# Performance work log

Hardware: AMD Instinct MI355X
Metric: run time of the kernel (lower is better)

The kernel has to match this reference:

```python
import jax, jax.numpy as jnp
import numpy as np

B = 64       # number of graphs
R = 148      # fixed ROI count from source
D = 64       # hidden_channels (embed_dim, 4 heads)
H = 4
IN1 = 64     # node feature dim (after stripping label column)
INR = 148    # roi-graph feature dim
HID = 1000
NCLS = 2
N1 = 262144
E1 = 1048576
N2 = B * R
E2 = 262144
EPS = 1e-5


def setup_inputs() -> dict:
    key = jax.random.key(0)
    ks = jax.random.split(key, 40)
    def p(i, shape, s=0.1):
        return jax.random.normal(ks[i], shape, dtype=jnp.float32) * s
    inp = {
        'x_feat': jax.random.normal(ks[0], (N1, IN1), dtype=jnp.float32),
        'node_roi': jax.random.randint(ks[1], (N1,), 0, R, dtype=jnp.int32),
        'batch1': ((jnp.arange(N1, dtype=jnp.int32) * B) // N1).astype(jnp.int32),
        'edge_index1': jax.random.randint(ks[2], (2, E1), 0, N1, dtype=jnp.int32),
        'edge_weight1': jax.random.uniform(ks[3], (E1,), dtype=jnp.float32, minval=0.1, maxval=1.0),
        'x2_feat': jax.random.normal(ks[4], (N2, INR), dtype=jnp.float32),
        'roi_labels2': (jnp.arange(N2, dtype=jnp.int32) % R).astype(jnp.int32),
        'batch2': (jnp.arange(N2, dtype=jnp.int32) // R).astype(jnp.int32),
        'edge_index2': jax.random.randint(ks[5], (2, E2), 0, N2, dtype=jnp.int32),
        'edge_weight2': jax.random.uniform(ks[6], (E2,), dtype=jnp.float32, minval=0.1, maxval=1.0),
        'Wg1': p(7, (IN1, D)), 'bg1': jnp.zeros((D,), jnp.float32),
        'Wg2': p(8, (D, D)), 'bg2': jnp.zeros((D,), jnp.float32),
        'Wr1': p(9, (INR, D)), 'br1': jnp.zeros((D,), jnp.float32),
        'Wr2': p(10, (D, D)), 'br2': jnp.zeros((D,), jnp.float32),
        'in_proj_w': p(11, (3 * D, D)), 'in_proj_b': jnp.zeros((3 * D,), jnp.float32),
        'out_proj_w': p(12, (D, D)), 'out_proj_b': jnp.zeros((D,), jnp.float32),
        'ln1_g': jnp.ones((D,), jnp.float32), 'ln1_b': jnp.zeros((D,), jnp.float32),
        'ff_w1': p(13, (D, D)), 'ff_b1': jnp.zeros((D,), jnp.float32),
        'ff_w2': p(14, (D, D)), 'ff_b2': jnp.zeros((D,), jnp.float32),
        'ln2_g': jnp.ones((D,), jnp.float32), 'ln2_b': jnp.zeros((D,), jnp.float32),
        'Wc1': p(15, (R * D, HID), 0.02), 'bc1': jnp.zeros((HID,), jnp.float32),
        'bn_g': jnp.ones((HID,), jnp.float32), 'bn_b': jnp.zeros((HID,), jnp.float32),
        'Wc2': p(16, (HID, NCLS), 0.02), 'bc2': jnp.zeros((NCLS,), jnp.float32),
    }
    return inp


def gcn_conv(h, src, dst, ew, W, b, n):
    # PyG GCNConv w/ edge weights: add self-loops (weight 1), sym-normalize.
    h = h @ W
    deg = jax.ops.segment_sum(ew, dst, num_segments=n) + 1.0
    dinv = jax.lax.rsqrt(deg)
    norm = dinv[src] * ew * dinv[dst]                      # (E,)
    agg = jax.ops.segment_sum(h[src] * norm[:, None], dst, num_segments=n)
    agg = agg + h * (dinv * dinv)[:, None]                 # self-loop term
    return agg + b


def roi_pool_mean(h, roi, batch):
    # fused scatter mean keyed by (batch, roi) -> (B, R, d); empty slots stay 0
    seg = batch * R + roi
    sums = jax.ops.segment_sum(h, seg, num_segments=B * R)
    cnt = jax.ops.segment_sum(jnp.ones_like(h[:, 0]), seg, num_segments=B * R)
    return (sums / jnp.maximum(cnt, 1.0)[:, None]).reshape(B, R, h.shape[1])


def layer_norm(x, g, b):
    mu = x.mean(axis=-1, keepdims=True)
    var = x.var(axis=-1, keepdims=True)
    return (x - mu) * jax.lax.rsqrt(var + EPS) * g + b


def reference(x_feat, node_roi, batch1, edge_index1, edge_weight1,
              x2_feat, roi_labels2, batch2, edge_index2, edge_weight2,
              Wg1, bg1, Wg2, bg2, Wr1, br1, Wr2, br2,
              in_proj_w, in_proj_b, out_proj_w, out_proj_b,
              ln1_g, ln1_b, ff_w1, ff_b1, ff_w2, ff_b2, ln2_g, ln2_b,
              Wc1, bc1, bn_g, bn_b, Wc2, bc2):
    s1, d1 = edge_index1[0], edge_index1[1]
    s2, d2 = edge_index2[0], edge_index2[1]

    # ROI-graph branch (convs_roi[:-1]): 2 GCN layers, relu, eval dropout=noop
    h2 = jax.nn.relu(gcn_conv(x2_feat, s2, d2, edge_weight2, Wr1, br1, N2))
    h2 = jax.nn.relu(gcn_conv(h2, s2, d2, edge_weight2, Wr2, br2, N2))
    pooled_roi = roi_pool_mean(h2, roi_labels2, batch2)          # (B,R,D)

    # node-graph branch (convs[:-1])
    h1 = jax.nn.relu(gcn_conv(x_feat, s1, d1, edge_weight1, Wg1, bg1, N1))
    h1 = jax.nn.relu(gcn_conv(h1, s1, d1, edge_weight1, Wg2, bg2, N1))
    pooled = roi_pool_mean(h1, node_roi, batch1)                 # (B,R,D)

    combined = pooled + pooled_roi                               # transformer_in_combined

    # SelfAttnBlock (torch MultiheadAttention, batch_first, 4 heads)
    hd = D // H
    qkv = combined @ in_proj_w.T + in_proj_b                     # (B,R,3D)
    q, k, v = jnp.split(qkv, 3, axis=-1)
    q = q.reshape(B, R, H, hd)
    k = k.reshape(B, R, H, hd)
    v = v.reshape(B, R, H, hd)
    scores = jnp.einsum('bqhd,bkhd->bhqk', q, k) / np.sqrt(hd).astype(np.float32)
    attn_w = jax.nn.softmax(scores, axis=-1)                     # (B,H,R,R)
    o = jnp.einsum('bhqk,bkhd->bqhd', attn_w, v).reshape(B, R, D)
    o = o @ out_proj_w.T + out_proj_b
    x = layer_norm(combined + o, ln1_g, ln1_b)
    f = jax.nn.relu(x @ ff_w1 + ff_b1) @ ff_w2 + ff_b2
    t_out = layer_norm(x + f, ln2_g, ln2_b)                      # (B,R,D)

    # classifier: Linear -> BatchNorm1d(eval: mean0,var1) -> LeakyReLU -> Linear
    z = t_out.reshape(B, R * D) @ Wc1 + bc1
    z = bn_g * z * jax.lax.rsqrt(jnp.asarray(1.0 + EPS, z.dtype)) + bn_b
    z = jnp.where(z >= 0, z, 0.01 * z)
    out = z @ Wc2 + bc2                                          # (B,NCLS)
    return (out, pooled, pooled_roi, t_out, attn_w)
```

## Files before the change

### kernel.cpp

```cpp
#include <hip/hip_runtime.h>
#include <cstdint>
#include <cstddef>

#define N1v 262144
#define E1v 1048576
#define N2v 9472
#define E2v 262144
#define BBv 64
#define RRv 148
#define HIDv 1000
#define BRv (BBv * RRv)
#define NSEG 9472
#define EPB 4096
#define NBK1 256
#define SH1 10
#define BINS1 1024
#define CAP1 4864
#define NBK2 74
#define SH2 7
#define BINS2 128
#define CAP2 4096

__host__ __device__ constexpr int cdiv(int a, int b) { return (a + b - 1) / b; }

typedef __attribute__((ext_vector_type(8))) short bf16x8;
typedef __attribute__((ext_vector_type(4))) float f32x4;
typedef unsigned short ushort_t;
typedef unsigned long long u64;

__device__ inline short f2bf(float f) {
    union { float f; unsigned u; } v; v.f = f;
    unsigned r = v.u + 0x7fff + ((v.u >> 16) & 1);
    return (short)(r >> 16);
}
__device__ inline float bf2f(unsigned hs) {
    union { unsigned u; float f; } v; v.u = hs << 16; return v.f;
}
__device__ inline unsigned relu_pk(unsigned u) {
    unsigned r = u;
    if (r & 0x8000u) r &= 0xFFFF0000u;
    if (r & 0x80000000u) r &= 0x0000FFFFu;
    return r;
}

__global__ __launch_bounds__(256) void k_binA(const int* __restrict__ dst1, int* __restrict__ bc1,
                                              const int* __restrict__ dst2, int* __restrict__ bc2) {
    int bid = blockIdx.x;
    const int* dst; int* bc; int nbk, sh, e0;
    if (bid < E1v / EPB) { dst = dst1; bc = bc1; nbk = NBK1; sh = SH1; e0 = bid * EPB; }
    else { dst = dst2; bc = bc2; nbk = NBK2; sh = SH2; e0 = (bid - E1v / EPB) * EPB; }
    __shared__ int h[256];
    int tid = threadIdx.x;
    if (tid < nbk) h[tid] = 0;
    __syncthreads();
    for (int t = tid; t < EPB; t += 256) atomicAdd(&h[dst[e0 + t] >> sh], 1);
    __syncthreads();
    if (tid < nbk && h[tid]) atomicAdd(&bc[tid], h[tid]);
}

__global__ __launch_bounds__(256) void k_scanAB(const int* __restrict__ bc1, int* __restrict__ bb1, int* __restrict__ cur1,
                                                const int* __restrict__ bc2, int* __restrict__ bb2, int* __restrict__ cur2) {
    __shared__ int tmp[256];
    int t = threadIdx.x;
    int v = bc1[t];
    tmp[t] = v; __syncthreads();
    int val = v;
    for (int off = 1; off < 256; off <<= 1) { int o = (t >= off) ? tmp[t - off] : 0; __syncthreads(); val += o; tmp[t] = val; __syncthreads(); }
    int excl = val - v;
    bb1[t] = excl; cur1[t] = excl;
    if (t == 255) bb1[256] = val;
    __syncthreads();
    int v2 = (t < NBK2) ? bc2[t] : 0;
    tmp[t] = v2; __syncthreads();
    int val2 = v2;
    for (int off = 1; off < 256; off <<= 1) { int o = (t >= off) ? tmp[t - off] : 0; __syncthreads(); val2 += o; tmp[t] = val2; __syncthreads(); }
    if (t < NBK2) { int e2 = val2 - v2; bb2[t] = e2; cur2[t] = e2; }
    if (t == NBK2 - 1) bb2[NBK2] = val2;
}

__global__ __launch_bounds__(256) void k_binB(const int* __restrict__ src1, const int* __restrict__ dst1,
                                              const float* __restrict__ ew1, int* __restrict__ cur1, u64* __restrict__ rb1,
                                              const int* __restrict__ src2, const int* __restrict__ dst2,
                                              const float* __restrict__ ew2, int* __restrict__ cur2, u64* __restrict__ rb2) {
    int bid = blockIdx.x;
    const int* src; const int* dst; const float* ew; int* cur; u64* rb; int nbk, sh, e0;
    if (bid < E1v / EPB) { src = src1; dst = dst1; ew = ew1; cur = cur1; rb = rb1; nbk = NBK1; sh = SH1; e0 = bid * EPB; }
    else { src = src2; dst = dst2; ew = ew2; cur = cur2; rb = rb2; nbk = NBK2; sh = SH2; e0 = (bid - E1v / EPB) * EPB; }
    __shared__ int h[256], basg[256];
    int tid = threadIdx.x;
    if (tid < nbk) h[tid] = 0;
    __syncthreads();
    for (int t = tid; t < EPB; t += 256) atomicAdd(&h[dst[e0 + t] >> sh], 1);
    __syncthreads();
    if (tid < nbk) {
        int c = h[tid];
        basg[tid] = c ? atomicAdd(&cur[tid], c) : 0;
        h[tid] = 0;
    }
    __syncthreads();
    unsigned lowmask = (1u << sh) - 1u;
    for (int t = tid; t < EPB; t += 256) {
        int d = dst[e0 + t];
        int b = d >> sh;
        int r = atomicAdd(&h[b], 1);
        unsigned lo = ((unsigned)src[e0 + t] << sh) | ((unsigned)d & lowmask);
        rb[(size_t)basg[b] + r] = ((u64)(unsigned)__float_as_int(ew[e0 + t]) << 32) | lo;
    }
}

template<int BINS, int CAP, int SH>
__global__ __launch_bounds__(256) void k_csrC(const u64* __restrict__ rb, const int* __restrict__ bb,
                                              float* __restrict__ dinv, int* __restrict__ offs,
                                              int2* __restrict__ snC) {
    int b = blockIdx.x;
    int beg = bb[b], end = bb[b + 1], cnt = end - beg;
    __shared__ int hist[BINS];
    __shared__ float degs[BINS];
    __shared__ int scn[BINS];
    __shared__ int tmp[256];
    extern __shared__ int2 outb[];
    int tid = threadIdx.x;
    for (int i = tid; i < BINS; i += 256) { hist[i] = 0; degs[i] = 0.f; }
    __syncthreads();
    for (int j = beg + tid; j < end; j += 256) {
        u64 rec = rb[j];
        int bin = (int)((unsigned)rec & (BINS - 1));
        float w = __int_as_float((int)(rec >> 32));
        atomicAdd(&hist[bin], 1);
        atomicAdd(&degs[bin], w);
    }
    __syncthreads();
    constexpr int PER = (BINS + 255) / 256;
    int lv[PER];
    int tsum = 0;
    int base_i = tid * PER;
#pragma unroll
    for (int k = 0; k < PER; ++k) { int idx = base_i + k; lv[k] = (idx < BINS) ? hist[idx] : 0; tsum += lv[k]; }
    tmp[tid] = tsum; __syncthreads();
    int val = tsum;
    for (int off = 1; off < 256; off <<= 1) { int o = (tid >= off) ? tmp[tid - off] : 0; __syncthreads(); val += o; tmp[tid] = val; __syncthreads(); }
    int run = val - tsum;
#pragma unroll
    for (int k = 0; k < PER; ++k) { int idx = base_i + k; if (idx < BINS) { scn[idx] = run; run += lv[k]; } }
    __syncthreads();
    for (int i = tid; i < BINS; i += 256) {
        offs[b * BINS + i] = beg + scn[i];
        dinv[b * BINS + i] = rsqrtf(degs[i] + 1.0f);
    }
    __syncthreads();
    bool staged = (cnt <= CAP);
    for (int j = beg + tid; j < end; j += 256) {
        u64 rec = rb[j];
        unsigned lo = (unsigned)rec;
        int bin = (int)(lo & (BINS - 1));
        int s = (int)(lo >> SH);
        int wbits = (int)(rec >> 32);
        int r = atomicAdd(&scn[bin], 1);
        int2 o2 = make_int2(s, wbits);
        if (staged) outb[r] = o2;
        else snC[(size_t)beg + r] = o2;
    }
    __syncthreads();
    if (staged) {
        for (int j = tid; j < cnt; j += 256) snC[(size_t)beg + j] = outb[j];
    }
}

__global__ __launch_bounds__(256) void k_pool_csr(const int* __restrict__ roi, int* __restrict__ offs_p,
                                                  int* __restrict__ nodeC) {
    int b = blockIdx.x;
    __shared__ int rl[4096];
    __shared__ int hist[RRv];
    __shared__ int curs[RRv];
    int tid = threadIdx.x;
    for (int t = tid; t < RRv; t += 256) hist[t] = 0;
    __syncthreads();
    int base = b * 4096;
    for (int t = tid; t < 4096; t += 256) {
        int r = roi[base + t];
        rl[t] = r;
        atomicAdd(&hist[r], 1);
    }
    __syncthreads();
    if (tid < RRv) {
        int s = 0;
        for (int k = 0; k < tid; ++k) s += hist[k];
        curs[tid] = s;
        offs_p[b * RRv + tid] = base + s;
    }
    __syncthreads();
    for (int t = tid; t < 4096; t += 256) {
        int r = rl[t];
        int j = atomicAdd(&curs[r], 1);
        nodeC[base + j] = base + t;
    }
}

__global__ __launch_bounds__(256) void k_pool_gather(const int* __restrict__ nodeC, const int* __restrict__ offs,
                                                     const ushort_t* __restrict__ Ab, float* __restrict__ pooled) {
    int tid = threadIdx.x;
    int lane = tid & 63;
    int nh = lane >> 5;
    int slot = (lane >> 3) & 3;
    int f8 = lane & 7;
    int gw = blockIdx.x * 4 + (tid >> 6);
    int tw = gridDim.x * 4;
    for (int ss = gw * 2; ss < NSEG; ss += tw * 2) {
        int s = ss + nh;
        int beg = offs[s];
        int end = (s + 1 < NSEG) ? offs[s + 1] : N1v;
        float a0 = 0.f, a1 = 0.f, a2 = 0.f, a3 = 0.f, a4 = 0.f, a5 = 0.f, a6 = 0.f, a7 = 0.f;
        for (int j = beg + slot; j < end; j += 4) {
            int node = nodeC[j];
            uint4 v = *(const uint4*)(Ab + (size_t)node * 64 + f8 * 8);
            a0 += fmaxf(bf2f(v.x & 0xffffu), 0.f);
            a1 += fmaxf(bf2f(v.x >> 16), 0.f);
            a2 += fmaxf(bf2f(v.y & 0xffffu), 0.f);
            a3 += fmaxf(bf2f(v.y >> 16), 0.f);
            a4 += fmaxf(bf2f(v.z & 0xffffu), 0.f);
            a5 += fmaxf(bf2f(v.z >> 16), 0.f);
            a6 += fmaxf(bf2f(v.w & 0xffffu), 0.f);
            a7 += fmaxf(bf2f(v.w >> 16), 0.f);
        }
        a0 += __shfl_xor(a0, 8);  a1 += __shfl_xor(a1, 8);  a2 += __shfl_xor(a2, 8);  a3 += __shfl_xor(a3, 8);
        a4 += __shfl_xor(a4, 8);  a5 += __shfl_xor(a5, 8);  a6 += __shfl_xor(a6, 8);  a7 += __shfl_xor(a7, 8);
        a0 += __shfl_xor(a0, 16); a1 += __shfl_xor(a1, 16); a2 += __shfl_xor(a2, 16); a3 += __shfl_xor(a3, 16);
        a4 += __shfl_xor(a4, 16); a5 += __shfl_xor(a5, 16); a6 += __shfl_xor(a6, 16); a7 += __shfl_xor(a7, 16);
        if (slot == 0) {
            float inv = 1.f / (float)max(end - beg, 1);
            float4 r0, r1;
            r0.x = a0 * inv; r0.y = a1 * inv; r0.z = a2 * inv; r0.w = a3 * inv;
            r1.x = a4 * inv; r1.y = a5 * inv; r1.z = a6 * inv; r1.w = a7 * inv;
            *(float4*)(pooled + (size_t)s * 64 + f8 * 8) = r0;
            *(float4*)(pooled + (size_t)s * 64 + f8 * 8 + 4) = r1;
        }
    }
}

__global__ __launch_bounds__(256) void k_edge_gather3(const int2* __restrict__ snC,
                                                      const int* __restrict__ offs, const ushort_t* __restrict__ Pb,
                                                      const float* __restrict__ dinv, const float* __restrict__ bias,
                                                      ushort_t* __restrict__ A, int N, int E) {
    int tid = threadIdx.x;
    int lane = tid & 63;
    int nh = lane >> 5;
    int slot = (lane >> 3) & 3;
    int f8 = lane & 7;
    float4 bv0 = *(const float4*)(bias + f8 * 8);
    float4 bv1 = *(const float4*)(bias + f8 * 8 + 4);
    int gw = blockIdx.x * 4 + (tid >> 6);
    int tw = gridDim.x * 4;
    for (int ii = gw * 2; ii < N; ii += tw * 2) {
        int i = ii + nh;
        int beg = offs[i];
        int end = (i + 1 < N) ? offs[i + 1] : E;
        float di = dinv[i];
        float a0 = 0.f, a1 = 0.f, a2 = 0.f, a3 = 0.f, a4 = 0.f, a5 = 0.f, a6 = 0.f, a7 = 0.f;
        for (int j = beg + slot; j < end; j += 4) {
            int2 e = snC[j];
            int s = e.x;
            float nv = dinv[s] * __int_as_float(e.y) * di;
            uint4 w = *(const uint4*)(Pb + (size_t)s * 64 + f8 * 8);
            a0 = fmaf(nv, bf2f(w.x & 0xffffu), a0);
            a1 = fmaf(nv, bf2f(w.x >> 16), a1);
            a2 = fmaf(nv, bf2f(w.y & 0xffffu), a2);
            a3 = fmaf(nv, bf2f(w.y >> 16), a3);
            a4 = fmaf(nv, bf2f(w.z & 0xffffu), a4);
            a5 = fmaf(nv, bf2f(w.z >> 16), a5);
            a6 = fmaf(nv, bf2f(w.w & 0xffffu), a6);
            a7 = fmaf(nv, bf2f(w.w >> 16), a7);
        }
        a0 += __shfl_xor(a0, 8);  a1 += __shfl_xor(a1, 8);  a2 += __shfl_xor(a2, 8);  a3 += __shfl_xor(a3, 8);
        a4 += __shfl_xor(a4, 8);  a5 += __shfl_xor(a5, 8);  a6 += __shfl_xor(a6, 8);  a7 += __shfl_xor(a7, 8);
        a0 += __shfl_xor(a0, 16); a1 += __shfl_xor(a1, 16); a2 += __shfl_xor(a2, 16); a3 += __shfl_xor(a3, 16);
        a4 += __shfl_xor(a4, 16); a5 += __shfl_xor(a5, 16); a6 += __shfl_xor(a6, 16); a7 += __shfl_xor(a7, 16);
        if (slot == 0) {
            uint4 w = *(const uint4*)(Pb + (size_t)i * 64 + f8 * 8);
            float s2 = di * di;
            float r0 = fmaf(s2, bf2f(w.x & 0xffffu), a0) + bv0.x;
            float r1 = fmaf(s2, bf2f(w.x >> 16),    a1) + bv0.y;
            float r2 = fmaf(s2, bf2f(w.y & 0xffffu), a2) + bv0.z;
            float r3 = fmaf(s2, bf2f(w.y >> 16),    a3) + bv0.w;
            float r4 = fmaf(s2, bf2f(w.z & 0xffffu), a4) + bv1.x;
            float r5 = fmaf(s2, bf2f(w.z >> 16),    a5) + bv1.y;
            float r6 = fmaf(s2, bf2f(w.w & 0xffffu), a6) + bv1.z;
            float r7 = fmaf(s2, bf2f(w.w >> 16),    a7) + bv1.w;
            uint4 ov;
            ov.x = (unsigned)(ushort_t)f2bf(r0) | ((unsigned)(ushort_t)f2bf(r1) << 16);
            ov.y = (unsigned)(ushort_t)f2bf(r2) | ((unsigned)(ushort_t)f2bf(r3) << 16);
            ov.z = (unsigned)(ushort_t)f2bf(r4) | ((unsigned)(ushort_t)f2bf(r5) << 16);
            ov.w = (unsigned)(ushort_t)f2bf(r6) | ((unsigned)(ushort_t)f2bf(r7) << 16);
            *(uint4*)(A + (size_t)i * 64 + f8 * 8) = ov;
        }
    }
}

template<bool RIN, bool IBF16>
__global__ __launch_bounds__(256) void k_gemm_mfma(const void* __restrict__ Xv, const float* __restrict__ Wmat,
                                                   ushort_t* __restrict__ Y, int N) {
    int tid = threadIdx.x;
    int lane = tid & 63;
    int wv = tid >> 6;
    int l15 = lane & 15;
    int lg = lane >> 4;
    bf16x8 bfrag[2][4];
    for (int kh = 0; kh < 2; ++kh)
        for (int ct = 0; ct < 4; ++ct) {
            bf16x8 b;
#pragma unroll
            for (int i = 0; i < 8; ++i)
                b[i] = f2bf(Wmat[(size_t)(kh * 32 + lg * 8 + i) * 64 + ct * 16 + l15]);
            bfrag[kh][ct] = b;
        }
    int gw = blockIdx.x * 4 + wv;
    int tw = gridDim.x * 4;
    int ntiles = N >> 4;
    for (int t = gw; t < ntiles; t += tw) {
        int row0 = t << 4;
        bf16x8 af0, af1;
        if (IBF16) {
            const ushort_t* xp = (const ushort_t*)Xv + (size_t)(row0 + l15) * 64 + lg * 8;
            uint4 c0 = *(const uint4*)(xp);
            uint4 c1 = *(const uint4*)(xp + 32);
            if (RIN) {
                c0.x = relu_pk(c0.x); c0.y = relu_pk(c0.y); c0.z = relu_pk(c0.z); c0.w = relu_pk(c0.w);
                c1.x = relu_pk(c1.x); c1.y = relu_pk(c1.y); c1.z = relu_pk(c1.z); c1.w = relu_pk(c1.w);
            }
            af0 = *reinterpret_cast<bf16x8*>(&c0);
            af1 = *reinterpret_cast<bf16x8*>(&c1);
        } else {
            const float* xp = (const float*)Xv + (size_t)(row0 + l15) * 64 + lg * 8;
            float4 a0 = *(const float4*)(xp);
            float4 a1 = *(const float4*)(xp + 4);
            float4 a2 = *(const float4*)(xp + 32);
            float4 a3 = *(const float4*)(xp + 36);
            if (RIN) {
                a0.x = fmaxf(a0.x, 0.f); a0.y = fmaxf(a0.y, 0.f); a0.z = fmaxf(a0.z, 0.f); a0.w = fmaxf(a0.w, 0.f);
                a1.x = fmaxf(a1.x, 0.f); a1.y = fmaxf(a1.y, 0.f); a1.z = fmaxf(a1.z, 0.f); a1.w = fmaxf(a1.w, 0.f);
                a2.x = fmaxf(a2.x, 0.f); a2.y = fmaxf(a2.y, 0.f); a2.z = fmaxf(a2.z, 0.f); a2.w = fmaxf(a2.w, 0.f);
                a3.x = fmaxf(a3.x, 0.f); a3.y = fmaxf(a3.y, 0.f); a3.z = fmaxf(a3.z, 0.f); a3.w = fmaxf(a3.w, 0.f);
            }
            af0[0] = f2bf(a0.x); af0[1] = f2bf(a0.y); af0[2] = f2bf(a0.z); af0[3] = f2bf(a0.w);
            af0[4] = f2bf(a1.x); af0[5] = f2bf(a1.y); af0[6] = f2bf(a1.z); af0[7] = f2bf(a1.w);
            af1[0] = f2bf(a2.x); af1[1] = f2bf(a2.y); af1[2] = f2bf(a2.z); af1[3] = f2bf(a2.w);
            af1[4] = f2bf(a3.x); af1[5] = f2bf(a3.y); af1[6] = f2bf(a3.z); af1[7] = f2bf(a3.w);
        }
        f32x4 acc0 = {0.f, 0.f, 0.f, 0.f}, acc1 = acc0, acc2 = acc0, acc3 = acc0;
        acc0 = __builtin_amdgcn_mfma_f32_16x16x32_bf16(af0, bfrag[0][0], acc0, 0, 0, 0);
        acc1 = __builtin_amdgcn_mfma_f32_16x16x32_bf16(af0, bfrag[0][1], acc1, 0, 0, 0);
        acc2 = __builtin_amdgcn_mfma_f32_16x16x32_bf16(af0, bfrag[0][2], acc2, 0, 0, 0);
        acc3 = __builtin_amdgcn_mfma_f32_16x16x32_bf16(af0, bfrag[0][3], acc3, 0, 0, 0);
        acc0 = __builtin_amdgcn_mfma_f32_16x16x32_bf16(af1, bfrag[1][0], acc0, 0, 0, 0);
        acc1 = __builtin_amdgcn_mfma_f32_16x16x32_bf16(af1, bfrag[1][1], acc1, 0, 0, 0);
        acc2 = __builtin_amdgcn_mfma_f32_16x16x32_bf16(af1, bfrag[1][2], acc2, 0, 0, 0);
        acc3 = __builtin_amdgcn_mfma_f32_16x16x32_bf16(af1, bfrag[1][3], acc3, 0, 0, 0);
        ushort_t* yp = Y + (size_t)(row0 + lg * 4) * 64 + l15;
#pragma unroll
        for (int r = 0; r < 4; ++r) {
            yp[(size_t)r * 64 + 0]  = (ushort_t)f2bf(acc0[r]);
            yp[(size_t)r * 64 + 16] = (ushort_t)f2bf(acc1[r]);
            yp[(size_t)r * 64 + 32] = (ushort_t)f2bf(acc2[r]);
            yp[(size_t)r * 64 + 48] = (ushort_t)f2bf(acc3[r]);
        }
    }
}

template<int MB, bool RIN, bool ROUT, bool OBF16>
__global__ __launch_bounds__(256) void k_gemm_rowwave(const float* __restrict__ X, const float* __restrict__ W,
                                                      const float* __restrict__ bias, void* __restrict__ Yv,
                                                      int N, int K) {
    extern __shared__ float Wl[];
    const int M = MB * 64;
    for (int idx = threadIdx.x; idx < K * M; idx += 256) Wl[idx] = W[idx];
    __syncthreads();
    int lane = threadIdx.x & 63;
    int gw = blockIdx.x * 4 + (threadIdx.x >> 6);
    int tw = gridDim.x * 4;
    const int K4 = K >> 2;
    for (int row = gw; row < N; row += tw) {
        float acc[MB];
#pragma unroll
        for (int cb = 0; cb < MB; ++cb) acc[cb] = 0.f;
        const float4* xr = (const float4*)(X + (size_t)row * K);
        for (int k4 = 0; k4 < K4; ++k4) {
            float4 xv = xr[k4];
            if (RIN) {
                xv.x = fmaxf(xv.x, 0.f); xv.y = fmaxf(xv.y, 0.f);
                xv.z = fmaxf(xv.z, 0.f); xv.w = fmaxf(xv.w, 0.f);
            }
            const float* wp = Wl + (k4 * 4) * M + lane;
#pragma unroll
            for (int cb = 0; cb < MB; ++cb) acc[cb] = fmaf(xv.x, wp[cb * 64], acc[cb]);
            wp += M;
#pragma unroll
            for (int cb = 0; cb < MB; ++cb) acc[cb] = fmaf(xv.y, wp[cb * 64], acc[cb]);
            wp += M;
#pragma unroll
            for (int cb = 0; cb < MB; ++cb) acc[cb] = fmaf(xv.z, wp[cb * 64], acc[cb]);
            wp += M;
#pragma unroll
            for (int cb = 0; cb < MB; ++cb) acc[cb] = fmaf(xv.w, wp[cb * 64], acc[cb]);
        }
#pragma unroll
        for (int cb = 0; cb < MB; ++cb) {
            float y = acc[cb];
            int col = cb * 64 + lane;
            if (bias) y += bias[col];
            if (ROUT) y = fmaxf(y, 0.f);
            if (OBF16) ((ushort_t*)Yv)[(size_t)row * M + col] = (ushort_t)f2bf(y);
            else ((float*)Yv)[(size_t)row * M + col] = y;
        }
    }
}

__global__ __launch_bounds__(256) void k_transpose2(const float* __restrict__ Win, float* __restrict__ WinT,
                                                    const float* __restrict__ Wout, float* __restrict__ WoutT) {
    int i = blockIdx.x * 256 + threadIdx.x;
    if (i < 192 * 64) {
        int r = i >> 6, c = i & 63;
        WinT[c * 192 + r] = Win[i];
    } else if (i < 192 * 64 + 64 * 64) {
        int j = i - 192 * 64;
        int r = j >> 6, c = j & 63;
        WoutT[c * 64 + r] = Wout[j];
    }
}

__global__ __launch_bounds__(256) void k_pool_fin2b(const ushort_t* __restrict__ h2Ab, const float* __restrict__ pooled,
                                                    float* __restrict__ pooledroi, float* __restrict__ comb,
                                                    int n4) {
    int i = blockIdx.x * 256 + threadIdx.x;
    if (i < n4) {
        uint2 v = *(const uint2*)(h2Ab + (size_t)i * 4);
        float4 p = ((const float4*)pooled)[i];
        float4 r;
        r.x = fmaxf(bf2f(v.x & 0xffffu), 0.f);
        r.y = fmaxf(bf2f(v.x >> 16), 0.f);
        r.z = fmaxf(bf2f(v.y & 0xffffu), 0.f);
        r.w = fmaxf(bf2f(v.y >> 16), 0.f);
        ((float4*)pooledroi)[i] = r;
        float4 c;
        c.x = r.x + p.x; c.y = r.y + p.y; c.z = r.z + p.z; c.w = r.w + p.w;
        ((float4*)comb)[i] = c;
    }
}

__global__ __launch_bounds__(256) void k_attn(const float* __restrict__ qkv, float* __restrict__ aw,
                                              float* __restrict__ o) {
    int qc = blockIdx.x & 3;
    int bh = blockIdx.x >> 2;
    int b = bh >> 2, h = bh & 3;
    __shared__ float qs[37][16];
    __shared__ float kT[16][152];
    __shared__ float vs[148][16];
    __shared__ float ps[4][152];
    int tid = threadIdx.x;
    const float* base = qkv + (size_t)b * 148 * 192 + h * 16;
    for (int idx = tid; idx < 148 * 16; idx += 256) {
        int i = idx >> 4, d = idx & 15;
        const float* p = base + (size_t)i * 192 + d;
        kT[d][i] = p[64];
        vs[i][d] = p[128];
    }
    int q0 = qc * 37;
    for (int idx = tid; idx < 37 * 16; idx += 256) {
        int i = idx >> 4, d = idx & 15;
        qs[i][d] = base[(size_t)(q0 + i) * 192 + d] * 0.25f;
    }
    __syncthreads();
    int wv = tid >> 6, lane = tid & 63;
    float* aw_bh = aw + (size_t)bh * 148 * 148;
    for (int ii = wv; ii < 37; ii += 4) {
        int i = q0 + ii;
        float s0 = 0.f, s1 = 0.f, s2 = 0.f;
#pragma unroll
        for (int d = 0; d < 16; ++d) {
            float q = qs[ii][d];
            s0 = fmaf(q, kT[d][lane], s0);
            s1 = fmaf(q, kT[d][lane + 64], s1);
            if (lane < 20) s2 = fmaf(q, kT[d][lane + 128], s2);
        }
        float m = fmaxf(s0, s1);
        if (lane < 20) m = fmaxf(m, s2);
#pragma unroll
        for (int off = 1; off < 64; off <<= 1) m = fmaxf(m, __shfl_xor(m, off));
        float e0 = __expf(s0 - m), e1 = __expf(s1 - m);
        float e2 = (lane < 20) ? __expf(s2 - m) : 0.f;
        float sum = e0 + e1 + e2;
#pragma unroll
        for (int off = 1; off < 64; off <<= 1) sum += __shfl_xor(sum, off);
        float inv = 1.f / sum;
        float p0 = e0 * inv, p1 = e1 * inv, p2 = e2 * inv;
        float* awr = aw_bh + (size_t)i * 148;
        awr[lane] = p0;
        awr[lane + 64] = p1;
        if (lane < 20) awr[lane + 128] = p2;
        ps[wv][lane] = p0;
        ps[wv][lane + 64] = p1;
        if (lane < 20) ps[wv][lane + 128] = p2;
        int d = lane & 15, jj = lane >> 4;
        float acc = 0.f;
        for (int t = jj; t < 148; t += 4) acc = fmaf(ps[wv][t], vs[t][d], acc);
        acc += __shfl_xor(acc, 16);
        acc += __shfl_xor(acc, 32);
        if (lane < 16) o[((size_t)b * 148 + i) * 64 + h * 16 + d] = acc;
    }
}

__global__ __launch_bounds__(256) void k_ln_gemm(const float* __restrict__ X, const float* __restrict__ Wt,
                                                 const float* __restrict__ bias, const float* __restrict__ resid,
                                                 const float* __restrict__ g, const float* __restrict__ bb,
                                                 float* __restrict__ Y, int N) {
    __shared__ float Wl[4096];
    for (int idx = threadIdx.x; idx < 4096; idx += 256) Wl[idx] = Wt[idx];
    __syncthreads();
    int lane = threadIdx.x & 63;
    int gw = blockIdx.x * 4 + (threadIdx.x >> 6);
    int tw = gridDim.x * 4;
    for (int row = gw; row < N; row += tw) {
        const float4* xr = (const float4*)(X + (size_t)row * 64);
        float acc = 0.f;
        for (int k4 = 0; k4 < 16; ++k4) {
            float4 xv = xr[k4];
            const float* wp = Wl + (k4 * 4) * 64 + lane;
            acc = fmaf(xv.x, wp[0], acc);
            acc = fmaf(xv.y, wp[64], acc);
            acc = fmaf(xv.z, wp[128], acc);
            acc = fmaf(xv.w, wp[192], acc);
        }
        float y = acc + bias[lane] + resid[(size_t)row * 64 + lane];
        float s = y;
#pragma unroll
        for (int off = 1; off < 64; off <<= 1) s += __shfl_xor(s, off);
        float mu = s * (1.f / 64.f);
        float dcen = y - mu;
        float v = dcen * dcen;
#pragma unroll
        for (int off = 1; off < 64; off <<= 1) v += __shfl_xor(v, off);
        float var = v * (1.f / 64.f);
        Y[(size_t)row * 64 + lane] = dcen * rsqrtf(var + 1e-5f) * g[lane] + bb[lane];
    }
}

__global__ __launch_bounds__(256) void k_cls_part(const float* __restrict__ T, const float* __restrict__ Wc1,
                                                  float* __restrict__ Zp) {
    int ks = blockIdx.x >> 2;
    int mt = blockIdx.x & 3;
    int k0 = ks * 74;
    int m0 = mt * 256;
    __shared__ float Tl[64][74];
    int tid = threadIdx.x;
    for (int idx = tid; idx < 64 * 74; idx += 256) {
        int b = idx / 74, kk = idx - b * 74;
        Tl[b][kk] = T[(size_t)b * 9472 + k0 + kk];
    }
    __syncthreads();
    int lane = tid & 63, bq = tid >> 6;
    int mbase = m0 + lane * 4;
    size_t moff = (mbase + 3 < 1000) ? (size_t)mbase : 0;
    float4 acc[16];
#pragma unroll
    for (int j = 0; j < 16; ++j) acc[j] = make_float4(0.f, 0.f, 0.f, 0.f);
#pragma unroll 2
    for (int kk = 0; kk < 74; ++kk) {
        float4 w = *(const float4*)(Wc1 + (size_t)(k0 + kk) * 1000 + moff);
#pragma unroll
        for (int j = 0; j < 16; ++j) {
            float t = Tl[bq * 16 + j][kk];
            acc[j].x = fmaf(t, w.x, acc[j].x);
            acc[j].y = fmaf(t, w.y, acc[j].y);
            acc[j].z = fmaf(t, w.z, acc[j].z);
            acc[j].w = fmaf(t, w.w, acc[j].w);
        }
    }
    float* zp = Zp + (size_t)ks * 64 * 1024;
#pragma unroll
    for (int j = 0; j < 16; ++j) {
        int b = bq * 16 + j;
        *(float4*)(zp + (size_t)b * 1024 + mbase) = acc[j];
    }
}

__global__ __launch_bounds__(256) void k_cls_reduce(const float* __restrict__ Zp, const float* __restrict__ bc1,
                                                    const float* __restrict__ bn_g, const float* __restrict__ bn_b,
                                                    float* __restrict__ zb) {
    int flat = blockIdx.x * 256 + threadIdx.x;
    int b = flat >> 10, m = flat & 1023;
    if (m >= 1000) return;
    float s = 0.f;
    for (int ks = 0; ks < 128; ++ks)
        s += Zp[((size_t)ks * 64 + b) * 1024 + m];
    float rs = rsqrtf(1.0f + 1e-5f);
    float z = bn_g[m] * (s + bc1[m]) * rs + bn_b[m];
    zb[flat] = z >= 0.f ? z : 0.01f * z;
}

__global__ __launch_bounds__(256) void k_cls_final(const float* __restrict__ zb,
                                                   const float* __restrict__ Wc2, const float* __restrict__ bc2,
                                                   float* __restrict__ out) {
    int b = blockIdx.x;
    int tid = threadIdx.x;
    float a0 = 0.f, a1 = 0.f;
    for (int m = tid; m < 1000; m += 256) {
        float z = zb[b * 1024 + m];
        a0 = fmaf(z, Wc2[m * 2], a0);
        a1 = fmaf(z, Wc2[m * 2 + 1], a1);
    }
#pragma unroll
    for (int off = 1; off < 64; off <<= 1) {
        a0 += __shfl_xor(a0, off);
        a1 += __shfl_xor(a1, off);
    }
    __shared__ float r0[4], r1[4];
    if ((tid & 63) == 0) { r0[tid >> 6] = a0; r1[tid >> 6] = a1; }
    __syncthreads();
    if (tid == 0) {
        out[b * 2 + 0] = r0[0] + r0[1] + r0[2] + r0[3] + bc2[0];
        out[b * 2 + 1] = r1[0] + r1[1] + r1[2] + r1[3] + bc2[1];
    }
}

extern "C" void kernel_launch(void* const* d_in, const int* in_sizes, int n_in,
                              void* d_out, int out_size, void* d_ws, size_t ws_size,
                              hipStream_t stream) {
    (void)in_sizes; (void)n_in; (void)out_size; (void)ws_size;

    const float* x_feat = (const float*)d_in[0];
    const int* node_roi = (const int*)d_in[1];
    const int* ei1 = (const int*)d_in[3];
    const float* ew1 = (const float*)d_in[4];
    const float* x2f = (const float*)d_in[5];
    const int* ei2 = (const int*)d_in[8];
    const float* ew2 = (const float*)d_in[9];
    const float* Wg1 = (const float*)d_in[10];
    const float* bg1 = (const float*)d_in[11];
    const float* Wg2 = (const float*)d_in[12];
    const float* bg2 = (const float*)d_in[13];
    const float* Wr1 = (const float*)d_in[14];
    const float* br1 = (const float*)d_in[15];
    const float* Wr2 = (const float*)d_in[16];
    const float* br2 = (const float*)d_in[17];
    const float* in_proj_w = (const float*)d_in[18];
    const float* in_proj_b = (const float*)d_in[19];
    const float* out_proj_w = (const float*)d_in[20];
    const float* out_proj_b = (const float*)d_in[21];
    const float* ln1_g = (const float*)d_in[22];
    const float* ln1_b = (const float*)d_in[23];
    const float* ff_w1 = (const float*)d_in[24];
    const float* ff_b1 = (const float*)d_in[25];
    const float* ff_w2 = (const float*)d_in[26];
    const float* ff_b2 = (const float*)d_in[27];
    const float* ln2_g = (const float*)d_in[28];
    const float* ln2_b = (const float*)d_in[29];
    const float* Wc1 = (const float*)d_in[30];
    const float* bc1 = (const float*)d_in[31];
    const float* bn_g = (const float*)d_in[32];
    const float* bn_b = (const float*)d_in[33];
    const float* Wc2 = (const float*)d_in[34];
    const float* bc2 = (const float*)d_in[35];

    const int* src1 = ei1;
    const int* dst1 = ei1 + E1v;
    const int* src2 = ei2;
    const int* dst2 = ei2 + E2v;

    float* out = (float*)d_out;
    const int PSZ = BRv * 64;
    float* pooled_out = out + 128;
    float* pooledroi_out = out + 128 + PSZ;
    float* tout_out = out + 128 + 2 * PSZ;
    float* attn_out = out + 128 + 3 * PSZ;

    float* W = (float*)d_ws;
    size_t o = 0;
    int* bcnt1 = (int*)(W + o);  o += 256;
    int* bcnt2 = (int*)(W + o);  o += 128;
    size_t zone_elems = o;
    int* bb1 = (int*)(W + o);  o += 260;
    int* cur1 = (int*)(W + o); o += 256;
    int* bb2 = (int*)(W + o);  o += 76;
    int* cur2 = (int*)(W + o); o += 128;
    o = (o + 1) & ~(size_t)1;
    int2* snC1 = (int2*)(W + o); o += (size_t)E1v * 2;
    int2* snC2 = (int2*)(W + o); o += (size_t)E2v * 2;
    float* dinv1 = W + o;        o += N1v;
    float* dinv2 = W + o;        o += N2v;
    int* offs1 = (int*)(W + o);  o += N1v;
    int* offs2 = (int*)(W + o);  o += N2v;
    int* offs_p = (int*)(W + o); o += NSEG;
    int* nodeC = (int*)(W + o);  o += N1v;
    float* zbuf = W + o;         o += BBv * 1024;
    o = (o + 1) & ~(size_t)1;
    size_t h1P_off = o; o += (size_t)N1v * 64;
    size_t h1A_off = o; o += (size_t)N1v * 64;
    ushort_t* h1P = (ushort_t*)(W + h1P_off);
    ushort_t* h1Ab = (ushort_t*)(W + h1A_off);
    u64* rb1 = (u64*)(W + h1P_off);
    u64* rb2 = rb1 + E1v;
    size_t p = h1P_off;
    ushort_t* h2P = (ushort_t*)(W + p);  p += (size_t)N2v * 64;
    ushort_t* h2Ab = (ushort_t*)(W + p); p += (size_t)N2v * 64;
    float* comb = W + p; p += PSZ;
    float* qkvb = W + p; p += (size_t)BRv * 192;
    float* obuf = W + p; p += PSZ;
    float* xbuf = W + p; p += PSZ;
    float* f1 = W + p;   p += PSZ;
    float* WinT = W + p; p += 64 * 192;
    float* WoutT = W + p; p += 64 * 64;
    float* Zp = W + h1A_off;

    dim3 blk(256);

    hipMemsetAsync(W, 0, zone_elems * sizeof(float), stream);

    k_binA<<<E1v / EPB + E2v / EPB, blk, 0, stream>>>(dst1, bcnt1, dst2, bcnt2);
    k_scanAB<<<1, blk, 0, stream>>>(bcnt1, bb1, cur1, bcnt2, bb2, cur2);
    k_binB<<<E1v / EPB + E2v / EPB, blk, 0, stream>>>(src1, dst1, ew1, cur1, rb1,
                                                      src2, dst2, ew2, cur2, rb2);
    k_csrC<BINS1, CAP1, SH1><<<NBK1, blk, CAP1 * 8, stream>>>(rb1, bb1, dinv1, offs1, snC1);
    k_csrC<BINS2, CAP2, SH2><<<NBK2, blk, CAP2 * 8, stream>>>(rb2, bb2, dinv2, offs2, snC2);
    k_pool_csr<<<BBv, blk, 0, stream>>>(node_roi, offs_p, nodeC);

    k_gemm_mfma<false, false><<<2048, blk, 0, stream>>>(x_feat, Wg1, h1P, N1v);
    k_edge_gather3<<<4096, blk, 0, stream>>>(snC1, offs1, h1P, dinv1, bg1, h1Ab, N1v, E1v);
    k_gemm_mfma<true, true><<<2048, blk, 0, stream>>>(h1Ab, Wg2, h1P, N1v);
    k_edge_gather3<<<4096, blk, 0, stream>>>(snC1, offs1, h1P, dinv1, bg2, h1Ab, N1v, E1v);
    k_pool_gather<<<2048, blk, 0, stream>>>(nodeC, offs_p, h1Ab, pooled_out);

    k_gemm_rowwave<1, false, false, true><<<cdiv(N2v, 4), blk, 148 * 64 * 4, stream>>>(x2f, Wr1, nullptr, h2P, N2v, 148);
    k_edge_gather3<<<cdiv(N2v, 8), blk, 0, stream>>>(snC2, offs2, h2P, dinv2, br1, h2Ab, N2v, E2v);
    k_gemm_mfma<true, true><<<148, blk, 0, stream>>>(h2Ab, Wr2, h2P, N2v);
    k_edge_gather3<<<cdiv(N2v, 8), blk, 0, stream>>>(snC2, offs2, h2P, dinv2, br2, h2Ab, N2v, E2v);
    k_pool_fin2b<<<cdiv(PSZ / 4, 256), blk, 0, stream>>>(h2Ab, pooled_out, pooledroi_out, comb, PSZ / 4);

    k_transpose2<<<cdiv(192 * 64 + 64 * 64, 256), blk, 0, stream>>>(in_proj_w, WinT, out_proj_w, WoutT);
    k_gemm_rowwave<3, false, false, false><<<cdiv(N2v, 4), blk, 64 * 192 * 4, stream>>>(comb, WinT, in_proj_b, qkvb, N2v, 64);
    k_attn<<<BBv * 4 * 4, blk, 0, stream>>>(qkvb, attn_out, obuf);
    k_ln_gemm<<<cdiv(N2v, 4), blk, 0, stream>>>(obuf, WoutT, out_proj_b, comb, ln1_g, ln1_b, xbuf, N2v);
    k_gemm_rowwave<1, false, true, false><<<cdiv(N2v, 4), blk, 64 * 64 * 4, stream>>>(xbuf, ff_w1, ff_b1, f1, N2v, 64);
    k_ln_gemm<<<cdiv(N2v, 4), blk, 0, stream>>>(f1, ff_w2, ff_b2, xbuf, ln2_g, ln2_b, tout_out, N2v);

    k_cls_part<<<512, blk, 0, stream>>>(tout_out, Wc1, Zp);
    k_cls_reduce<<<BBv * 1024 / 256, blk, 0, stream>>>(Zp, bc1, bn_g, bn_b, zbuf);
    k_cls_final<<<BBv, blk, 0, stream>>>(zbuf, Wc2, bc2, out);
}
```

Measured before the change: 435.0 us.

## Prefold GCN edge normalization and co-launch both graph branches in merged kernels

Edge weights in the sorted CSR are pre-multiplied by dinv[dst] in the CSR builder and by dinv[src] in a new normfix pass. This removes the per-edge dinv[s] random load and multiply from every gather. The gather and bf16 GEMM stages of the large node graph and the ROI graph are now horizontally fused into single launches that split work by block index, and the ROI pooling/combine step is folded into the node pooling kernel. The h2 buffers move out of the aliased h1 region so both branches can run together. The cost is one extra read-write pass over all edges and larger workspace use.

```diff
diff --git a/kernel.cpp b/kernel.cpp
--- a/kernel.cpp
+++ b/kernel.cpp
@@ -20,6 +20,10 @@
 #define SH2 7
 #define BINS2 128
 #define CAP2 4096
+#define GB1 4096
+#define GB2 1184
+#define MB1 2048
+#define MB2 148
 
 __host__ __device__ constexpr int cdiv(int a, int b) { return (a + b - 1) / b; }
 
@@ -154,9 +158,10 @@
         unsigned lo = (unsigned)rec;
         int bin = (int)(lo & (BINS - 1));
         int s = (int)(lo >> SH);
-        int wbits = (int)(rec >> 32);
+        float w = __int_as_float((int)(rec >> 32));
+        float wd = w * rsqrtf(degs[bin] + 1.0f);
         int r = atomicAdd(&scn[bin], 1);
-        int2 o2 = make_int2(s, wbits);
+        int2 o2 = make_int2(s, __float_as_int(wd));
         if (staged) outb[r] = o2;
         else snC[(size_t)beg + r] = o2;
     }
@@ -164,6 +169,17 @@
     if (staged) {
         for (int j = tid; j < cnt; j += 256) snC[(size_t)beg + j] = outb[j];
     }
+}
+
+__global__ __launch_bounds__(256) void k_normfix(int2* __restrict__ snC1, const float* __restrict__ dinv1,
+                                                 int2* __restrict__ snC2, const float* __restrict__ dinv2) {
+    int bid = blockIdx.x;
+    int2* snC; const float* dinv; int j;
+    if (bid < E1v / 256) { snC = snC1; dinv = dinv1; j = bid * 256 + threadIdx.x; }
+    else { snC = snC2; dinv = dinv2; j = (bid - E1v / 256) * 256 + threadIdx.x; }
+    int2 e = snC[j];
+    e.y = __float_as_int(dinv[e.x] * __int_as_float(e.y));
+    snC[j] = e;
 }
 
 __global__ __launch_bounds__(256) void k_pool_csr(const int* __restrict__ roi, int* __restrict__ offs_p,
@@ -196,8 +212,10 @@
     }
 }
 
-__global__ __launch_bounds__(256) void k_pool_gather(const int* __restrict__ nodeC, const int* __restrict__ offs,
-                                                     const ushort_t* __restrict__ Ab, float* __restrict__ pooled) {
+__global__ __launch_bounds__(256) void k_pool_all(const int* __restrict__ nodeC, const int* __restrict__ offs,
+                                                  const ushort_t* __restrict__ Ab, const ushort_t* __restrict__ h2Ab,
+                                                  float* __restrict__ pooled, float* __restrict__ pooledroi,
+                                                  float* __restrict__ comb) {
     int tid = threadIdx.x;
     int lane = tid & 63;
     int nh = lane >> 5;
@@ -228,38 +246,47 @@
         a4 += __shfl_xor(a4, 16); a5 += __shfl_xor(a5, 16); a6 += __shfl_xor(a6, 16); a7 += __shfl_xor(a7, 16);
         if (slot == 0) {
             float inv = 1.f / (float)max(end - beg, 1);
-            float4 r0, r1;
-            r0.x = a0 * inv; r0.y = a1 * inv; r0.z = a2 * inv; r0.w = a3 * inv;
-            r1.x = a4 * inv; r1.y = a5 * inv; r1.z = a6 * inv; r1.w = a7 * inv;
-            *(float4*)(pooled + (size_t)s * 64 + f8 * 8) = r0;
-            *(float4*)(pooled + (size_t)s * 64 + f8 * 8 + 4) = r1;
-        }
-    }
-}
-
-__global__ __launch_bounds__(256) void k_edge_gather3(const int2* __restrict__ snC,
-                                                      const int* __restrict__ offs, const ushort_t* __restrict__ Pb,
-                                                      const float* __restrict__ dinv, const float* __restrict__ bias,
-                                                      ushort_t* __restrict__ A, int N, int E) {
-    int tid = threadIdx.x;
-    int lane = tid & 63;
+            float p0 = a0 * inv, p1 = a1 * inv, p2 = a2 * inv, p3 = a3 * inv;
+            float p4 = a4 * inv, p5 = a5 * inv, p6 = a6 * inv, p7 = a7 * inv;
+            uint4 v2 = *(const uint4*)(h2Ab + (size_t)s * 64 + f8 * 8);
+            float q0 = fmaxf(bf2f(v2.x & 0xffffu), 0.f);
+            float q1 = fmaxf(bf2f(v2.x >> 16), 0.f);
+            float q2 = fmaxf(bf2f(v2.y & 0xffffu), 0.f);
+            float q3 = fmaxf(bf2f(v2.y >> 16), 0.f);
+            float q4 = fmaxf(bf2f(v2.z & 0xffffu), 0.f);
+            float q5 = fmaxf(bf2f(v2.z >> 16), 0.f);
+            float q6 = fmaxf(bf2f(v2.w & 0xffffu), 0.f);
+            float q7 = fmaxf(bf2f(v2.w >> 16), 0.f);
+            size_t bo = (size_t)s * 64 + f8 * 8;
+            float4 t;
+            t.x = p0; t.y = p1; t.z = p2; t.w = p3; *(float4*)(pooled + bo) = t;
+            t.x = p4; t.y = p5; t.z = p6; t.w = p7; *(float4*)(pooled + bo + 4) = t;
+            t.x = q0; t.y = q1; t.z = q2; t.w = q3; *(float4*)(pooledroi + bo) = t;
+            t.x = q4; t.y = q5; t.z = q6; t.w = q7; *(float4*)(pooledroi + bo + 4) = t;
+            t.x = p0 + q0; t.y = p1 + q1; t.z = p2 + q2; t.w = p3 + q3; *(float4*)(comb + bo) = t;
+            t.x = p4 + q4; t.y = p5 + q5; t.z = p6 + q6; t.w = p7 + q7; *(float4*)(comb + bo + 4) = t;
+        }
+    }
+}
+
+__device__ inline void gather_body(const int2* __restrict__ snC, const int* __restrict__ offs,
+                                   const ushort_t* __restrict__ Pb, const float* __restrict__ dinv,
+                                   const float* __restrict__ bias, ushort_t* __restrict__ A,
+                                   int N, int E, int gw, int tw, int lane) {
     int nh = lane >> 5;
     int slot = (lane >> 3) & 3;
     int f8 = lane & 7;
     float4 bv0 = *(const float4*)(bias + f8 * 8);
     float4 bv1 = *(const float4*)(bias + f8 * 8 + 4);
-    int gw = blockIdx.x * 4 + (tid >> 6);
-    int tw = gridDim.x * 4;
     for (int ii = gw * 2; ii < N; ii += tw * 2) {
         int i = ii + nh;
         int beg = offs[i];
         int end = (i + 1 < N) ? offs[i + 1] : E;
-        float di = dinv[i];
         float a0 = 0.f, a1 = 0.f, a2 = 0.f, a3 = 0.f, a4 = 0.f, a5 = 0.f, a6 = 0.f, a7 = 0.f;
         for (int j = beg + slot; j < end; j += 4) {
             int2 e = snC[j];
             int s = e.x;
-            float nv = dinv[s] * __int_as_float(e.y) * di;
+            float nv = __int_as_float(e.y);
             uint4 w = *(const uint4*)(Pb + (size_t)s * 64 + f8 * 8);
             a0 = fmaf(nv, bf2f(w.x & 0xffffu), a0);
             a1 = fmaf(nv, bf2f(w.x >> 16), a1);
@@ -276,6 +303,7 @@
         a4 += __shfl_xor(a4, 16); a5 += __shfl_xor(a5, 16); a6 += __shfl_xor(a6, 16); a7 += __shfl_xor(a7, 16);
         if (slot == 0) {
             uint4 w = *(const uint4*)(Pb + (size_t)i * 64 + f8 * 8);
+            float di = dinv[i];
             float s2 = di * di;
             float r0 = fmaf(s2, bf2f(w.x & 0xffffu), a0) + bv0.x;
             float r1 = fmaf(s2, bf2f(w.x >> 16),    a1) + bv0.y;
@@ -295,12 +323,25 @@
     }
 }
 
-template<bool RIN, bool IBF16>
-__global__ __launch_bounds__(256) void k_gemm_mfma(const void* __restrict__ Xv, const float* __restrict__ Wmat,
-                                                   ushort_t* __restrict__ Y, int N) {
+__global__ __launch_bounds__(256) void k_gather_both(const int2* __restrict__ snC1, const int* __restrict__ offs1,
+                                                     const ushort_t* __restrict__ P1, const float* __restrict__ dinv1,
+                                                     const float* __restrict__ b1, ushort_t* __restrict__ A1,
+                                                     const int2* __restrict__ snC2, const int* __restrict__ offs2,
+                                                     const ushort_t* __restrict__ P2, const float* __restrict__ dinv2,
+                                                     const float* __restrict__ b2, ushort_t* __restrict__ A2) {
     int tid = threadIdx.x;
     int lane = tid & 63;
-    int wv = tid >> 6;
+    if (blockIdx.x < GB1)
+        gather_body(snC1, offs1, P1, dinv1, b1, A1, N1v, E1v,
+                    blockIdx.x * 4 + (tid >> 6), GB1 * 4, lane);
+    else
+        gather_body(snC2, offs2, P2, dinv2, b2, A2, N2v, E2v,
+                    (blockIdx.x - GB1) * 4 + (tid >> 6), GB2 * 4, lane);
+}
+
+__device__ inline void gemm_bf16_body(const ushort_t* __restrict__ X, const float* __restrict__ Wmat,
+                                      ushort_t* __restrict__ Y, int N, int gw, int tw, int tid) {
+    int lane = tid & 63;
     int l15 = lane & 15;
     int lg = lane >> 4;
     bf16x8 bfrag[2][4];
@@ -312,39 +353,16 @@
                 b[i] = f2bf(Wmat[(size_t)(kh * 32 + lg * 8 + i) * 64 + ct * 16 + l15]);
             bfrag[kh][ct] = b;
         }
-    int gw = blockIdx.x * 4 + wv;
-    int tw = gridDim.x * 4;
     int ntiles = N >> 4;
     for (int t = gw; t < ntiles; t += tw) {
         int row0 = t << 4;
-        bf16x8 af0, af1;
-        if (IBF16) {
-            const ushort_t* xp = (const ushort_t*)Xv + (size_t)(row0 + l15) * 64 + lg * 8;
-            uint4 c0 = *(const uint4*)(xp);
-            uint4 c1 = *(const uint4*)(xp + 32);
-            if (RIN) {
-                c0.x = relu_pk(c0.x); c0.y = relu_pk(c0.y); c0.z = relu_pk(c0.z); c0.w = relu_pk(c0.w);
-                c1.x = relu_pk(c1.x); c1.y = relu_pk(c1.y); c1.z = relu_pk(c1.z); c1.w = relu_pk(c1.w);
-            }
-            af0 = *reinterpret_cast<bf16x8*>(&c0);
-            af1 = *reinterpret_cast<bf16x8*>(&c1);
-        } else {
-            const float* xp = (const float*)Xv + (size_t)(row0 + l15) * 64 + lg * 8;
-            float4 a0 = *(const float4*)(xp);
-            float4 a1 = *(const float4*)(xp + 4);
-            float4 a2 = *(const float4*)(xp + 32);
-            float4 a3 = *(const float4*)(xp + 36);
-            if (RIN) {
-                a0.x = fmaxf(a0.x, 0.f); a0.y = fmaxf(a0.y, 0.f); a0.z = fmaxf(a0.z, 0.f); a0.w = fmaxf(a0.w, 0.f);
-                a1.x = fmaxf(a1.x, 0.f); a1.y = fmaxf(a1.y, 0.f); a1.z = fmaxf(a1.z, 0.f); a1.w = fmaxf(a1.w, 0.f);
-                a2.x = fmaxf(a2.x, 0.f); a2.y = fmaxf(a2.y, 0.f); a2.z = fmaxf(a2.z, 0.f); a2.w = fmaxf(a2.w, 0.f);
-                a3.x = fmaxf(a3.x, 0.f); a3.y = fmaxf(a3.y, 0.f); a3.z = fmaxf(a3.z, 0.f); a3.w = fmaxf(a3.w, 0.f);
-            }
-            af0[0] = f2bf(a0.x); af0[1] = f2bf(a0.y); af0[2] = f2bf(a0.z); af0[3] = f2bf(a0.w);
-            af0[4] = f2bf(a1.x); af0[5] = f2bf(a1.y); af0[6] = f2bf(a1.z); af0[7] = f2bf(a1.w);
-            af1[0] = f2bf(a2.x); af1[1] = f2bf(a2.y); af1[2] = f2bf(a2.z); af1[3] = f2bf(a2.w);
-            af1[4] = f2bf(a3.x); af1[5] = f2bf(a3.y); af1[6] = f2bf(a3.z); af1[7] = f2bf(a3.w);
-        }
+        const ushort_t* xp = X + (size_t)(row0 + l15) * 64 + lg * 8;
+        uint4 c0 = *(const uint4*)(xp);
+        uint4 c1 = *(const uint4*)(xp + 32);
+        c0.x = relu_pk(c0.x); c0.y = relu_pk(c0.y); c0.z = relu_pk(c0.z); c0.w = relu_pk(c0.w);
+        c1.x = relu_pk(c1.x); c1.y = relu_pk(c1.y); c1.z = relu_pk(c1.z); c1.w = relu_pk(c1.w);
+        bf16x8 af0 = *reinterpret_cast<bf16x8*>(&c0);
+        bf16x8 af1 = *reinterpret_cast<bf16x8*>(&c1);
         f32x4 acc0 = {0.f, 0.f, 0.f, 0.f}, acc1 = acc0, acc2 = acc0, acc3 = acc0;
         acc0 = __builtin_amdgcn_mfma_f32_16x16x32_bf16(af0, bfrag[0][0], acc0, 0, 0, 0);
         acc1 = __builtin_amdgcn_mfma_f32_16x16x32_bf16(af0, bfrag[0][1], acc1, 0, 0, 0);
@@ -365,6 +383,68 @@
     }
 }
 
+__global__ __launch_bounds__(256) void k_gemm_both(const ushort_t* __restrict__ X1, const float* __restrict__ W1,
+                                                   ushort_t* __restrict__ Y1,
+                                                   const ushort_t* __restrict__ X2, const float* __restrict__ W2,
+                                                   ushort_t* __restrict__ Y2) {
+    int tid = threadIdx.x;
+    if (blockIdx.x < MB1)
+        gemm_bf16_body(X1, W1, Y1, N1v, blockIdx.x * 4 + (tid >> 6), MB1 * 4, tid);
+    else
+        gemm_bf16_body(X2, W2, Y2, N2v, (blockIdx.x - MB1) * 4 + (tid >> 6), MB2 * 4, tid);
+}
+
+__global__ __launch_bounds__(256) void k_gemm_mfma_f32(const float* __restrict__ X, const float* __restrict__ Wmat,
+                                                       ushort_t* __restrict__ Y, int N) {
+    int tid = threadIdx.x;
+    int lane = tid & 63;
+    int wv = tid >> 6;
+    int l15 = lane & 15;
+    int lg = lane >> 4;
+    bf16x8 bfrag[2][4];
+    for (int kh = 0; kh < 2; ++kh)
+        for (int ct = 0; ct < 4; ++ct) {
+            bf16x8 b;
+#pragma unroll
+            for (int i = 0; i < 8; ++i)
+                b[i] = f2bf(Wmat[(size_t)(kh * 32 + lg * 8 + i) * 64 + ct * 16 + l15]);
+            bfrag[kh][ct] = b;
+        }
+    int gw = blockIdx.x * 4 + wv;
+    int tw = gridDim.x * 4;
+    int ntiles = N >> 4;
+    for (int t = gw; t < ntiles; t += tw) {
+        int row0 = t << 4;
+        const float* xp = X + (size_t)(row0 + l15) * 64 + lg * 8;
+        float4 a0 = *(const float4*)(xp);
+        float4 a1 = *(const float4*)(xp + 4);
+        float4 a2 = *(const float4*)(xp + 32);
+        float4 a3 = *(const float4*)(xp + 36);
+        bf16x8 af0, af1;
+        af0[0] = f2bf(a0.x); af0[1] = f2bf(a0.y); af0[2] = f2bf(a0.z); af0[3] = f2bf(a0.w);
+        af0[4] = f2bf(a1.x); af0[5] = f2bf(a1.y); af0[6] = f2bf(a1.z); af0[7] = f2bf(a1.w);
+        af1[0] = f2bf(a2.x); af1[1] = f2bf(a2.y); af1[2] = f2bf(a2.z); af1[3] = f2bf(a2.w);
+        af1[4] = f2bf(a3.x); af1[5] = f2bf(a3.y); af1[6] = f2bf(a3.z); af1[7] = f2bf(a3.w);
+        f32x4 acc0 = {0.f, 0.f, 0.f, 0.f}, acc1 = acc0, acc2 = acc0, acc3 = acc0;
+        acc0 = __builtin_amdgcn_mfma_f32_16x16x32_bf16(af0, bfrag[0][0], acc0, 0, 0, 0);
+        acc1 = __builtin_amdgcn_mfma_f32_16x16x32_bf16(af0, bfrag[0][1], acc1, 0, 0, 0);
+        acc2 = __builtin_amdgcn_mfma_f32_16x16x32_bf16(af0, bfrag[0][2], acc2, 0, 0, 0);
+        acc3 = __builtin_amdgcn_mfma_f32_16x16x32_bf16(af0, bfrag[0][3], acc3, 0, 0, 0);
+        acc0 = __builtin_amdgcn_mfma_f32_16x16x32_bf16(af1, bfrag[1][0], acc0, 0, 0, 0);
+        acc1 = __builtin_amdgcn_mfma_f32_16x16x32_bf16(af1, bfrag[1][1], acc1, 0, 0, 0);
+        acc2 = __builtin_amdgcn_mfma_f32_16x16x32_bf16(af1, bfrag[1][2], acc2, 0, 0, 0);
+        acc3 = __builtin_amdgcn_mfma_f32_16x16x32_bf16(af1, bfrag[1][3], acc3, 0, 0, 0);
+        ushort_t* yp = Y + (size_t)(row0 + lg * 4) * 64 + l15;
+#pragma unroll
+        for (int r = 0; r < 4; ++r) {
+            yp[(size_t)r * 64 + 0]  = (ushort_t)f2bf(acc0[r]);
+            yp[(size_t)r * 64 + 16] = (ushort_t)f2bf(acc1[r]);
+            yp[(size_t)r * 64 + 32] = (ushort_t)f2bf(acc2[r]);
+            yp[(size_t)r * 64 + 48] = (ushort_t)f2bf(acc3[r]);
+        }
+    }
+}
+
 template<int MB, bool RIN, bool ROUT, bool OBF16>
 __global__ __launch_bounds__(256) void k_gemm_rowwave(const float* __restrict__ X, const float* __restrict__ W,
                                                       const float* __restrict__ bias, void* __restrict__ Yv,
@@ -423,25 +503,6 @@
         int j = i - 192 * 64;
         int r = j >> 6, c = j & 63;
         WoutT[c * 64 + r] = Wout[j];
-    }
-}
-
-__global__ __launch_bounds__(256) void k_pool_fin2b(const ushort_t* __restrict__ h2Ab, const float* __restrict__ pooled,
-                                                    float* __restrict__ pooledroi, float* __restrict__ comb,
-                                                    int n4) {
-    int i = blockIdx.x * 256 + threadIdx.x;
-    if (i < n4) {
-        uint2 v = *(const uint2*)(h2Ab + (size_t)i * 4);
-        float4 p = ((const float4*)pooled)[i];
-        float4 r;
-        r.x = fmaxf(bf2f(v.x & 0xffffu), 0.f);
-        r.y = fmaxf(bf2f(v.x >> 16), 0.f);
-        r.z = fmaxf(bf2f(v.y & 0xffffu), 0.f);
-        r.w = fmaxf(bf2f(v.y >> 16), 0.f);
-        ((float4*)pooledroi)[i] = r;
-        float4 c;
-        c.x = r.x + p.x; c.y = r.y + p.y; c.z = r.z + p.z; c.w = r.w + p.w;
-        ((float4*)comb)[i] = c;
     }
 }
 
@@ -691,6 +752,9 @@
     int* nodeC = (int*)(W + o);  o += N1v;
     float* zbuf = W + o;         o += BBv * 1024;
     o = (o + 1) & ~(size_t)1;
+    ushort_t* h2P = (ushort_t*)(W + o);  o += (size_t)N2v * 32;
+    ushort_t* h2Ab = (ushort_t*)(W + o); o += (size_t)N2v * 32;
+    o = (o + 1) & ~(size_t)1;
     size_t h1P_off = o; o += (size_t)N1v * 64;
     size_t h1A_off = o; o += (size_t)N1v * 64;
     ushort_t* h1P = (ushort_t*)(W + h1P_off);
@@ -698,8 +762,6 @@
     u64* rb1 = (u64*)(W + h1P_off);
     u64* rb2 = rb1 + E1v;
     size_t p = h1P_off;
-    ushort_t* h2P = (ushort_t*)(W + p);  p += (size_t)N2v * 64;
-    ushort_t* h2Ab = (ushort_t*)(W + p); p += (size_t)N2v * 64;
     float* comb = W + p; p += PSZ;
     float* qkvb = W + p; p += (size_t)BRv * 192;
     float* obuf = W + p; p += PSZ;
@@ -719,19 +781,17 @@
                                                       src2, dst2, ew2, cur2, rb2);
     k_csrC<BINS1, CAP1, SH1><<<NBK1, blk, CAP1 * 8, stream>>>(rb1, bb1, dinv1, offs1, snC1);
     k_csrC<BINS2, CAP2, SH2><<<NBK2, blk, CAP2 * 8, stream>>>(rb2, bb2, dinv2, offs2, snC2);
+    k_normfix<<<E1v / 256 + E2v / 256, blk, 0, stream>>>(snC1, dinv1, snC2, dinv2);
     k_pool_csr<<<BBv, blk, 0, stream>>>(node_roi, offs_p, nodeC);
 
-    k_gemm_mfma<false, false><<<2048, blk, 0, stream>>>(x_feat, Wg1, h1P, N1v);
-    k_edge_gather3<<<4096, blk, 0, stream>>>(snC1, offs1, h1P, dinv1, bg1, h1Ab, N1v, E1v);
-    k_gemm_mfma<true, true><<<2048, blk, 0, stream>>>(h1Ab, Wg2, h1P, N1v);
-    k_edge_gather3<<<4096, blk, 0, stream>>>(snC1, offs1, h1P, dinv1, bg2, h1Ab, N1v, E1v);
-    k_pool_gather<<<2048, blk, 0, stream>>>(nodeC, offs_p, h1Ab, pooled_out);
-
+    k_gemm_mfma_f32<<<MB1, blk, 0, stream>>>(x_feat, Wg1, h1P, N1v);
     k_gemm_rowwave<1, false, false, true><<<cdiv(N2v, 4), blk, 148 * 64 * 4, stream>>>(x2f, Wr1, nullptr, h2P, N2v, 148);
-    k_edge_gather3<<<cdiv(N2v, 8), blk, 0, stream>>>(snC2, offs2, h2P, dinv2, br1, h2Ab, N2v, E2v);
-    k_gemm_mfma<true, true><<<148, blk, 0, stream>>>(h2Ab, Wr2, h2P, N2v);
-    k_edge_gather3<<<cdiv(N2v, 8), blk, 0, stream>>>(snC2, offs2, h2P, dinv2, br2, h2Ab, N2v, E2v);
-    k_pool_fin2b<<<cdiv(PSZ / 4, 256), blk, 0, stream>>>(h2Ab, pooled_out, pooledroi_out, comb, PSZ / 4);
+    k_gather_both<<<GB1 + GB2, blk, 0, stream>>>(snC1, offs1, h1P, dinv1, bg1, h1Ab,
+                                                 snC2, offs2, h2P, dinv2, br1, h2Ab);
+    k_gemm_both<<<MB1 + MB2, blk, 0, stream>>>(h1Ab, Wg2, h1P, h2Ab, Wr2, h2P);
+    k_gather_both<<<GB1 + GB2, blk, 0, stream>>>(snC1, offs1, h1P, dinv1, bg2, h1Ab,
+                                                 snC2, offs2, h2P, dinv2, br2, h2Ab);
+    k_pool_all<<<2048, blk, 0, stream>>>(nodeC, offs_p, h1Ab, h2Ab, pooled_out, pooledroi_out, comb);
 
     k_transpose2<<<cdiv(192 * 64 + 64 * 64, 256), blk, 0, stream>>>(in_proj_w, WinT, out_proj_w, WoutT);
     k_gemm_rowwave<3, false, false, false><<<cdiv(N2v, 4), blk, 64 * 192 * 4, stream>>>(comb, WinT, in_proj_b, qkvb, N2v, 64);
```

After: 421.6 us. -3.1%, faster.
